# Kernel optimization log

Hardware: AMD Instinct MI355X
Metric: run time of the kernel (lower is better)

## Reference

```python
import jax, jax.numpy as jnp
import numpy as np

LN_EPS = 1e-5

def setup_inputs() -> dict:
    key = jax.random.key(0)
    ks = jax.random.split(key, 8)
    E, N, D, H = 600000, 50000, 128, 512
    edge_attr = jax.random.normal(ks[0], (E, D), dtype=jnp.float32)
    node_feat_src = jax.random.normal(ks[1], (N, D), dtype=jnp.float32)
    node_feat_dst = jax.random.normal(ks[2], (N, D), dtype=jnp.float32)
    edge_index = jax.random.randint(ks[3], (2, E), 0, N, dtype=jnp.int64)
    in_dim = D + 2 * D  # 384
    W1 = jax.random.normal(ks[4], (in_dim, H), dtype=jnp.float32) / np.sqrt(in_dim)
    b1 = jnp.zeros((H,), dtype=jnp.float32)
    g1 = jnp.ones((H,), dtype=jnp.float32)
    be1 = jnp.zeros((H,), dtype=jnp.float32)
    W2 = jax.random.normal(ks[5], (H, D), dtype=jnp.float32) / np.sqrt(H)
    b2 = jnp.zeros((D,), dtype=jnp.float32)
    return dict(edge_attr=edge_attr, node_feat_src=node_feat_src,
                node_feat_dst=node_feat_dst, edge_index=edge_index,
                W1=W1, b1=b1, g1=g1, be1=be1, W2=W2, b2=b2)

def _layer_norm(x, gamma, beta):
    mu = jnp.mean(x, axis=-1, keepdims=True)
    var = jnp.mean(jnp.square(x - mu), axis=-1, keepdims=True)
    return (x - mu) * jax.lax.rsqrt(var + LN_EPS) * gamma + beta

def reference(edge_attr, node_feat_src, node_feat_dst, edge_index,
              W1, b1, g1, be1, W2, b2):
    src_idx, dst_idx = edge_index[0], edge_index[1]
    src_feat = node_feat_src[src_idx]            # [E, node_dim] gather
    dst_feat = node_feat_dst[dst_idx]            # [E, node_dim] gather
    x = jnp.concatenate([edge_attr, src_feat, dst_feat], axis=-1)  # [E, 3D]
    h = x @ W1 + b1                              # [E, H]
    h = jax.nn.silu(_layer_norm(h, g1, be1))
    out = h @ W2 + b2                            # [E, edge_dim]
    return edge_attr + out
```

## Files before the change

### kernel.cpp

```cpp
#include <hip/hip_runtime.h>
#include <hip/hip_bf16.h>


#define E_TOTAL 600000
#define DD      128
#define HH      512
#define IND     384
#define MTILE   64
#define XS      520

typedef __attribute__((ext_vector_type(8))) short bf16x8;
typedef __attribute__((ext_vector_type(4))) float f32x4;

__device__ __forceinline__ ushort f2bf(float f) {
    __hip_bfloat16 b = __float2bfloat16(f);
    return *reinterpret_cast<ushort*>(&b);
}

template <int CTRL>
__device__ __forceinline__ float dpp_add(float x) {
    union { float f; int i; } a, b;
    a.f = x;
    b.i = __builtin_amdgcn_update_dpp(0, a.i, CTRL, 0xf, 0xf, true);
    return x + b.f;
}
__device__ __forceinline__ float row16_sum(float s) {
    s = dpp_add<0xB1>(s);
    s = dpp_add<0x4E>(s);
    s = dpp_add<0x124>(s);
    s = dpp_add<0x128>(s);
    return s;
}

__global__ void prep_weights(const float* __restrict__ W1, const float* __restrict__ W2,
                             ushort* __restrict__ W1t, ushort* __restrict__ W2t) {
    int j = blockIdx.x * 256 + threadIdx.x;
    if (j < IND * HH) {
        int n = j / IND, k = j % IND;
        W1t[j] = f2bf(W1[k * HH + n]);
    }
    int j2 = j - IND * HH;
    if (j2 >= 0 && j2 < HH * DD) {
        int d2 = j2 / HH, k = j2 % HH;
        W2t[j2] = f2bf(W2[k * DD + d2]);
    }
}

__global__ __launch_bounds__(512, 4) void edge_block_kernel(
    const float* __restrict__ edge_attr,
    const float* __restrict__ nsrc,
    const float* __restrict__ ndst,
    const int*   __restrict__ eidx,
    const float* __restrict__ b1,
    const float* __restrict__ g1,
    const float* __restrict__ be1,
    const float* __restrict__ b2,
    const ushort* __restrict__ W1t,
    const ushort* __restrict__ W2t,
    float* __restrict__ out)
{
    __shared__ __align__(16) ushort xbuf[MTILE * XS];
    __shared__ float red_s[MTILE][8];
    __shared__ float red_q[MTILE][8];
    __shared__ __align__(8) float stats[MTILE][2];

    const int tid  = threadIdx.x;
    const int e0   = blockIdx.x * MTILE;
    const int lane = tid & 63;
    const int w    = tid >> 6;
    const int g    = lane >> 4;
    const int li   = lane & 15;

    {
        const int l32 = tid & 31, grp = tid >> 5;
        int si[4], di[4];
        #pragma unroll
        for (int it = 0; it < 4; ++it) {
            const int e = e0 + grp + it * 16;
            si[it] = eidx[e];
            di[it] = eidx[E_TOTAL + e];
        }
        #pragma unroll
        for (int it = 0; it < 4; ++it) {
            const int r = grp + it * 16;
            const int e = e0 + r;
            float4 ea = *(const float4*)&edge_attr[(size_t)e * DD + l32 * 4];
            float4 sf = *(const float4*)&nsrc[(size_t)si[it] * DD + l32 * 4];
            float4 df = *(const float4*)&ndst[(size_t)di[it] * DD + l32 * 4];
            ushort* row = &xbuf[r * XS];
            ushort4 ua = { f2bf(ea.x), f2bf(ea.y), f2bf(ea.z), f2bf(ea.w) };
            ushort4 us = { f2bf(sf.x), f2bf(sf.y), f2bf(sf.z), f2bf(sf.w) };
            ushort4 ud = { f2bf(df.x), f2bf(df.y), f2bf(df.z), f2bf(df.w) };
            *(ushort4*)&row[  0 + l32 * 4] = ua;
            *(ushort4*)&row[128 + l32 * 4] = us;
            *(ushort4*)&row[256 + l32 * 4] = ud;
        }
    }
    __syncthreads();

    const int wn0 = w * 64;
    f32x4 acc[4][4];
    #pragma unroll
    for (int mi = 0; mi < 4; ++mi)
        #pragma unroll
        for (int ni = 0; ni < 4; ++ni)
            acc[mi][ni] = (f32x4){0.f, 0.f, 0.f, 0.f};

    const ushort* w1p = W1t + (size_t)(wn0 + li) * IND + g * 8;

    bf16x8 B1b[2][4];
    #pragma unroll
    for (int ni = 0; ni < 4; ++ni) B1b[0][ni] = *(const bf16x8*)(w1p + ni * 16 * IND);
    #pragma unroll
    for (int ni = 0; ni < 4; ++ni) B1b[1][ni] = *(const bf16x8*)(w1p + ni * 16 * IND + 32);

    #pragma unroll
    for (int kb = 0; kb < 12; ++kb) {
        const int cur = kb & 1;
        const int ko  = kb * 32 + g * 8;
        bf16x8 a[4];
        #pragma unroll
        for (int mi = 0; mi < 4; ++mi)
            a[mi] = *(const bf16x8*)&xbuf[(mi * 16 + li) * XS + ko];
        __builtin_amdgcn_s_setprio(1);
        #pragma unroll
        for (int mi = 0; mi < 4; ++mi)
            #pragma unroll
            for (int ni = 0; ni < 4; ++ni)
                acc[mi][ni] = __builtin_amdgcn_mfma_f32_16x16x32_bf16(
                    a[mi], B1b[cur][ni], acc[mi][ni], 0, 0, 0);
        __builtin_amdgcn_s_setprio(0);
        if (kb < 10) {
            #pragma unroll
            for (int ni = 0; ni < 4; ++ni)
                B1b[cur][ni] = *(const bf16x8*)(w1p + ni * 16 * IND + (kb + 2) * 32);
        }
    }

    float b1v[4], g1v[4], bev[4];
    #pragma unroll
    for (int ni = 0; ni < 4; ++ni) {
        int c = wn0 + ni * 16 + li;
        b1v[ni] = b1[c]; g1v[ni] = g1[c]; bev[ni] = be1[c];
    }

    #pragma unroll
    for (int mi = 0; mi < 4; ++mi) {
        #pragma unroll
        for (int reg = 0; reg < 4; ++reg) {
            float s = 0.f, q = 0.f;
            #pragma unroll
            for (int ni = 0; ni < 4; ++ni) {
                float h = acc[mi][ni][reg] + b1v[ni];
                acc[mi][ni][reg] = h;
                s += h;
                q = fmaf(h, h, q);
            }
            s = row16_sum(s);
            q = row16_sum(q);
            if (li == 0) {
                int row = mi * 16 + g * 4 + reg;
                red_s[row][w] = s;
                red_q[row][w] = q;
            }
        }
    }
    __syncthreads();

    if (tid < MTILE) {
        float s = 0.f, q = 0.f;
        #pragma unroll
        for (int i = 0; i < 8; ++i) { s += red_s[tid][i]; q += red_q[tid][i]; }
        float mu  = s * (1.f / 512.f);
        float var = q * (1.f / 512.f) - mu * mu;
        stats[tid][0] = mu;
        stats[tid][1] = rsqrtf(var + 1e-5f);
    }
    __syncthreads();

    const ushort* w2p = W2t + (size_t)(w * 16 + li) * HH + g * 8;
    bf16x8 B2r[4];
    #pragma unroll
    for (int i = 0; i < 4; ++i) B2r[i] = *(const bf16x8*)(w2p + i * 32);

    #pragma unroll
    for (int mi = 0; mi < 4; ++mi) {
        #pragma unroll
        for (int reg = 0; reg < 4; ++reg) {
            int row = mi * 16 + g * 4 + reg;
            float2 st = *(float2*)&stats[row][0];
            #pragma unroll
            for (int ni = 0; ni < 4; ++ni) {
                float sc = st.y * g1v[ni];
                float tc = fmaf(-st.x, sc, bev[ni]);
                float xn = fmaf(acc[mi][ni][reg], sc, tc);
                float ex = __expf(-xn);
                float a  = xn * __builtin_amdgcn_rcpf(1.f + ex);
                xbuf[row * XS + wn0 + ni * 16 + li] = f2bf(a);
            }
        }
    }
    __syncthreads();

    float ear[8];
    #pragma unroll
    for (int mi = 0; mi < 2; ++mi)
        #pragma unroll
        for (int reg = 0; reg < 4; ++reg) {
            int row = (mi * 2) * 16 + g * 4 + reg;
            ear[mi * 4 + reg] = 0.f;
        }
    float earr[4][4];
    #pragma unroll
    for (int mi = 0; mi < 4; ++mi)
        #pragma unroll
        for (int reg = 0; reg < 4; ++reg) {
            int row = mi * 16 + g * 4 + reg;
            earr[mi][reg] = edge_attr[(size_t)(e0 + row) * DD + w * 16 + li];
        }

    f32x4 acc2[4];
    #pragma unroll
    for (int mi = 0; mi < 4; ++mi) acc2[mi] = (f32x4){0.f, 0.f, 0.f, 0.f};

    #pragma unroll
    for (int kb = 0; kb < 16; ++kb) {
        const int cur = kb & 3;
        bf16x8 bf = B2r[cur];
        if (kb < 12)
            B2r[cur] = *(const bf16x8*)(w2p + (kb + 4) * 32);
        const int ko = kb * 32 + g * 8;
        bf16x8 a2[4];
        #pragma unroll
        for (int mi = 0; mi < 4; ++mi)
            a2[mi] = *(const bf16x8*)&xbuf[(mi * 16 + li) * XS + ko];
        __builtin_amdgcn_s_setprio(1);
        #pragma unroll
        for (int mi = 0; mi < 4; ++mi)
            acc2[mi] = __builtin_amdgcn_mfma_f32_16x16x32_bf16(a2[mi], bf, acc2[mi], 0, 0, 0);
        __builtin_amdgcn_s_setprio(0);
    }

    const float b2v = b2[w * 16 + li];
    #pragma unroll
    for (int mi = 0; mi < 4; ++mi) {
        #pragma unroll
        for (int reg = 0; reg < 4; ++reg) {
            int row = mi * 16 + g * 4 + reg;
            size_t o = (size_t)(e0 + row) * DD + w * 16 + li;
            out[o] = acc2[mi][reg] + b2v + earr[mi][reg];
        }
    }
    (void)ear;
}

extern "C" void kernel_launch(void* const* d_in, const int* in_sizes, int n_in,
                              void* d_out, int out_size, void* d_ws, size_t ws_size,
                              hipStream_t stream) {
    const float* edge_attr = (const float*)d_in[0];
    const float* nsrc      = (const float*)d_in[1];
    const float* ndst      = (const float*)d_in[2];
    const int*   eidx      = (const int*)d_in[3];
    const float* W1        = (const float*)d_in[4];
    const float* b1        = (const float*)d_in[5];
    const float* g1        = (const float*)d_in[6];
    const float* be1       = (const float*)d_in[7];
    const float* W2        = (const float*)d_in[8];
    const float* b2        = (const float*)d_in[9];
    float* out = (float*)d_out;

    ushort* W1t = (ushort*)d_ws;
    ushort* W2t = W1t + IND * HH;

    hipLaunchKernelGGL(prep_weights,
                       dim3((IND * HH + HH * DD + 255) / 256), dim3(256), 0, stream,
                       W1, W2, W1t, W2t);

    hipLaunchKernelGGL(edge_block_kernel,
                       dim3(E_TOTAL / MTILE), dim3(512), 0, stream,
                       edge_attr, nsrc, ndst, eidx, b1, g1, be1, b2, W1t, W2t, out);
}
```

Measured before the change: 665.4 us.

## Switch both GEMMs to 32x32x16 MFMA with a 2x4 warp tiling

Replaces the 16x16x32 bf16 MFMA tiles with 32x32x16 tiles and reorganises the 8 waves into a 2x4 (M x N) grid. Each wave now computes 32 rows by 128 columns in GEMM1 and 32 rows by 32 columns in GEMM2, with A fragments double-buffered from LDS. The intent is fewer LDS reads per FLOP and higher MFMA efficiency. The LayerNorm reduction indexing and the output mapping are rewritten to match the new accumulator layout, which carries a risk of indexing errors. Lowering the per-wave tile to 32 rows also changes how much the W2 fragment loads are reused.

```diff
diff --git a/kernel.cpp b/kernel.cpp
--- a/kernel.cpp
+++ b/kernel.cpp
@@ -9,8 +9,8 @@
 #define MTILE   64
 #define XS      520
 
-typedef __attribute__((ext_vector_type(8))) short bf16x8;
-typedef __attribute__((ext_vector_type(4))) float f32x4;
+typedef __attribute__((ext_vector_type(8)))  short bf16x8;
+typedef __attribute__((ext_vector_type(16))) float f32x16;
 
 __device__ __forceinline__ ushort f2bf(float f) {
     __hip_bfloat16 b = __float2bfloat16(f);
@@ -68,8 +68,11 @@
     const int e0   = blockIdx.x * MTILE;
     const int lane = tid & 63;
     const int w    = tid >> 6;
-    const int g    = lane >> 4;
-    const int li   = lane & 15;
+    const int l31  = lane & 31;
+    const int hi   = lane >> 5;
+    const int hi2  = (lane >> 4) & 1;
+    const int wm   = w >> 2;
+    const int wn   = w & 3;
 
     {
         const int l32 = tid & 31, grp = tid >> 5;
@@ -98,71 +101,65 @@
     }
     __syncthreads();
 
-    const int wn0 = w * 64;
-    f32x4 acc[4][4];
-    #pragma unroll
-    for (int mi = 0; mi < 4; ++mi)
-        #pragma unroll
-        for (int ni = 0; ni < 4; ++ni)
-            acc[mi][ni] = (f32x4){0.f, 0.f, 0.f, 0.f};
-
-    const ushort* w1p = W1t + (size_t)(wn0 + li) * IND + g * 8;
-
-    bf16x8 B1b[2][4];
-    #pragma unroll
-    for (int ni = 0; ni < 4; ++ni) B1b[0][ni] = *(const bf16x8*)(w1p + ni * 16 * IND);
-    #pragma unroll
-    for (int ni = 0; ni < 4; ++ni) B1b[1][ni] = *(const bf16x8*)(w1p + ni * 16 * IND + 32);
-
-    #pragma unroll
-    for (int kb = 0; kb < 12; ++kb) {
-        const int cur = kb & 1;
-        const int ko  = kb * 32 + g * 8;
-        bf16x8 a[4];
-        #pragma unroll
-        for (int mi = 0; mi < 4; ++mi)
-            a[mi] = *(const bf16x8*)&xbuf[(mi * 16 + li) * XS + ko];
+    f32x16 acc[4];
+    #pragma unroll
+    for (int nf = 0; nf < 4; ++nf)
+        #pragma unroll
+        for (int r = 0; r < 16; ++r) acc[nf][r] = 0.f;
+
+    const ushort* w1p = W1t + (size_t)(wn * 128 + l31) * IND + hi * 8;
+    const ushort* xrow = &xbuf[(wm * 32 + l31) * XS + hi * 8];
+
+    bf16x8 B1r[2][4];
+    #pragma unroll
+    for (int nf = 0; nf < 4; ++nf) B1r[0][nf] = *(const bf16x8*)(w1p + nf * 32 * IND);
+    #pragma unroll
+    for (int nf = 0; nf < 4; ++nf) B1r[1][nf] = *(const bf16x8*)(w1p + nf * 32 * IND + 16);
+
+    bf16x8 a_[2];
+    a_[0] = *(const bf16x8*)(xrow);
+
+    #pragma unroll
+    for (int ks = 0; ks < 24; ++ks) {
+        const int cur = ks & 1;
+        if (ks < 23)
+            a_[cur ^ 1] = *(const bf16x8*)(xrow + (ks + 1) * 16);
         __builtin_amdgcn_s_setprio(1);
         #pragma unroll
-        for (int mi = 0; mi < 4; ++mi)
+        for (int nf = 0; nf < 4; ++nf)
+            acc[nf] = __builtin_amdgcn_mfma_f32_32x32x16_bf16(
+                a_[cur], B1r[cur][nf], acc[nf], 0, 0, 0);
+        __builtin_amdgcn_s_setprio(0);
+        if (ks < 22) {
             #pragma unroll
-            for (int ni = 0; ni < 4; ++ni)
-                acc[mi][ni] = __builtin_amdgcn_mfma_f32_16x16x32_bf16(
-                    a[mi], B1b[cur][ni], acc[mi][ni], 0, 0, 0);
-        __builtin_amdgcn_s_setprio(0);
-        if (kb < 10) {
-            #pragma unroll
-            for (int ni = 0; ni < 4; ++ni)
-                B1b[cur][ni] = *(const bf16x8*)(w1p + ni * 16 * IND + (kb + 2) * 32);
+            for (int nf = 0; nf < 4; ++nf)
+                B1r[cur][nf] = *(const bf16x8*)(w1p + nf * 32 * IND + (ks + 2) * 16);
         }
     }
 
     float b1v[4], g1v[4], bev[4];
     #pragma unroll
-    for (int ni = 0; ni < 4; ++ni) {
-        int c = wn0 + ni * 16 + li;
-        b1v[ni] = b1[c]; g1v[ni] = g1[c]; bev[ni] = be1[c];
-    }
-
-    #pragma unroll
-    for (int mi = 0; mi < 4; ++mi) {
-        #pragma unroll
-        for (int reg = 0; reg < 4; ++reg) {
-            float s = 0.f, q = 0.f;
-            #pragma unroll
-            for (int ni = 0; ni < 4; ++ni) {
-                float h = acc[mi][ni][reg] + b1v[ni];
-                acc[mi][ni][reg] = h;
-                s += h;
-                q = fmaf(h, h, q);
-            }
-            s = row16_sum(s);
-            q = row16_sum(q);
-            if (li == 0) {
-                int row = mi * 16 + g * 4 + reg;
-                red_s[row][w] = s;
-                red_q[row][w] = q;
-            }
+    for (int nf = 0; nf < 4; ++nf) {
+        int c = wn * 128 + nf * 32 + l31;
+        b1v[nf] = b1[c]; g1v[nf] = g1[c]; bev[nf] = be1[c];
+    }
+
+    #pragma unroll
+    for (int reg = 0; reg < 16; ++reg) {
+        float s = 0.f, q = 0.f;
+        #pragma unroll
+        for (int nf = 0; nf < 4; ++nf) {
+            float h = acc[nf][reg] + b1v[nf];
+            acc[nf][reg] = h;
+            s += h;
+            q = fmaf(h, h, q);
+        }
+        s = row16_sum(s);
+        q = row16_sum(q);
+        if ((lane & 15) == 0) {
+            int row = wm * 32 + (reg & 3) + 8 * (reg >> 2) + 4 * hi;
+            red_s[row][wn * 2 + hi2] = s;
+            red_q[row][wn * 2 + hi2] = q;
         }
     }
     __syncthreads();
@@ -178,80 +175,59 @@
     }
     __syncthreads();
 
-    const ushort* w2p = W2t + (size_t)(w * 16 + li) * HH + g * 8;
+    #pragma unroll
+    for (int reg = 0; reg < 16; ++reg) {
+        int row = wm * 32 + (reg & 3) + 8 * (reg >> 2) + 4 * hi;
+        float2 st = *(float2*)&stats[row][0];
+        #pragma unroll
+        for (int nf = 0; nf < 4; ++nf) {
+            float sc = st.y * g1v[nf];
+            float tc = fmaf(-st.x, sc, bev[nf]);
+            float xn = fmaf(acc[nf][reg], sc, tc);
+            float av = xn * __builtin_amdgcn_rcpf(1.f + __expf(-xn));
+            xbuf[row * XS + wn * 128 + nf * 32 + l31] = f2bf(av);
+        }
+    }
+
+    float earr[16];
+    #pragma unroll
+    for (int reg = 0; reg < 16; ++reg) {
+        int row = wm * 32 + (reg & 3) + 8 * (reg >> 2) + 4 * hi;
+        earr[reg] = edge_attr[(size_t)(e0 + row) * DD + wn * 32 + l31];
+    }
+    __syncthreads();
+
+    const ushort* w2p = W2t + (size_t)(wn * 32 + l31) * HH + hi * 8;
+    const ushort* arow2 = &xbuf[(wm * 32 + l31) * XS + hi * 8];
+
     bf16x8 B2r[4];
     #pragma unroll
-    for (int i = 0; i < 4; ++i) B2r[i] = *(const bf16x8*)(w2p + i * 32);
-
-    #pragma unroll
-    for (int mi = 0; mi < 4; ++mi) {
-        #pragma unroll
-        for (int reg = 0; reg < 4; ++reg) {
-            int row = mi * 16 + g * 4 + reg;
-            float2 st = *(float2*)&stats[row][0];
-            #pragma unroll
-            for (int ni = 0; ni < 4; ++ni) {
-                float sc = st.y * g1v[ni];
-                float tc = fmaf(-st.x, sc, bev[ni]);
-                float xn = fmaf(acc[mi][ni][reg], sc, tc);
-                float ex = __expf(-xn);
-                float a  = xn * __builtin_amdgcn_rcpf(1.f + ex);
-                xbuf[row * XS + wn0 + ni * 16 + li] = f2bf(a);
-            }
-        }
-    }
-    __syncthreads();
-
-    float ear[8];
-    #pragma unroll
-    for (int mi = 0; mi < 2; ++mi)
-        #pragma unroll
-        for (int reg = 0; reg < 4; ++reg) {
-            int row = (mi * 2) * 16 + g * 4 + reg;
-            ear[mi * 4 + reg] = 0.f;
-        }
-    float earr[4][4];
-    #pragma unroll
-    for (int mi = 0; mi < 4; ++mi)
-        #pragma unroll
-        for (int reg = 0; reg < 4; ++reg) {
-            int row = mi * 16 + g * 4 + reg;
-            earr[mi][reg] = edge_attr[(size_t)(e0 + row) * DD + w * 16 + li];
-        }
-
-    f32x4 acc2[4];
-    #pragma unroll
-    for (int mi = 0; mi < 4; ++mi) acc2[mi] = (f32x4){0.f, 0.f, 0.f, 0.f};
-
-    #pragma unroll
-    for (int kb = 0; kb < 16; ++kb) {
-        const int cur = kb & 3;
-        bf16x8 bf = B2r[cur];
-        if (kb < 12)
-            B2r[cur] = *(const bf16x8*)(w2p + (kb + 4) * 32);
-        const int ko = kb * 32 + g * 8;
-        bf16x8 a2[4];
-        #pragma unroll
-        for (int mi = 0; mi < 4; ++mi)
-            a2[mi] = *(const bf16x8*)&xbuf[(mi * 16 + li) * XS + ko];
-        __builtin_amdgcn_s_setprio(1);
-        #pragma unroll
-        for (int mi = 0; mi < 4; ++mi)
-            acc2[mi] = __builtin_amdgcn_mfma_f32_16x16x32_bf16(a2[mi], bf, acc2[mi], 0, 0, 0);
-        __builtin_amdgcn_s_setprio(0);
-    }
-
-    const float b2v = b2[w * 16 + li];
-    #pragma unroll
-    for (int mi = 0; mi < 4; ++mi) {
-        #pragma unroll
-        for (int reg = 0; reg < 4; ++reg) {
-            int row = mi * 16 + g * 4 + reg;
-            size_t o = (size_t)(e0 + row) * DD + w * 16 + li;
-            out[o] = acc2[mi][reg] + b2v + earr[mi][reg];
-        }
-    }
-    (void)ear;
+    for (int i = 0; i < 4; ++i) B2r[i] = *(const bf16x8*)(w2p + i * 16);
+
+    f32x16 acc2;
+    #pragma unroll
+    for (int r = 0; r < 16; ++r) acc2[r] = 0.f;
+
+    bf16x8 a2_[2];
+    a2_[0] = *(const bf16x8*)(arow2);
+
+    #pragma unroll
+    for (int ks = 0; ks < 32; ++ks) {
+        const int cur = ks & 1;
+        if (ks < 31)
+            a2_[cur ^ 1] = *(const bf16x8*)(arow2 + (ks + 1) * 16);
+        acc2 = __builtin_amdgcn_mfma_f32_32x32x16_bf16(a2_[cur], B2r[ks & 3], acc2, 0, 0, 0);
+        if (ks < 28)
+            B2r[ks & 3] = *(const bf16x8*)(w2p + (ks + 4) * 16);
+    }
+
+    const float b2v = b2[wn * 32 + l31];
+    #pragma unroll
+    for (int reg = 0; reg < 16; ++reg) {
+        int row = wm * 32 + (reg & 3) + 8 * (reg >> 2) + 4 * hi;
+        size_t o = (size_t)(e0 + row) * DD + wn * 32 + l31;
+        out[o] = acc2[reg] + b2v + earr[reg];
+    }
 }
 
 extern "C" void kernel_launch(void* const* d_in, const int* in_sizes, int n_in,
```

Result: slower. 1.214 ms (+82.5%).

## Replace padded LDS rows with XOR-swizzled layout and hoist epilogue loads

Applied to the files above, without the earlier changes.

The padded shared-memory row stride (520) is replaced by unpadded rows of 384 (first GEMM) and 512 (second GEMM), using an XOR swizzle of 8-element chunks keyed on the row to avoid bank conflicts. This cuts LDS footprint from 66.5KB to 64KB per block, which may ease occupancy. The edge_attr residual loads and W2 fragment prefetch are moved earlier, before the LayerNorm reduction barrier, so their latency overlaps the stats computation. Swizzle indexing adds some integer ALU work and must stay consistent between writers and readers.

```diff
diff --git a/kernel.cpp b/kernel.cpp
--- a/kernel.cpp
+++ b/kernel.cpp
@@ -7,7 +7,6 @@
 #define HH      512
 #define IND     384
 #define MTILE   64
-#define XS      520
 
 typedef __attribute__((ext_vector_type(8))) short bf16x8;
 typedef __attribute__((ext_vector_type(4))) float f32x4;
@@ -59,7 +58,7 @@
     const ushort* __restrict__ W2t,
     float* __restrict__ out)
 {
-    __shared__ __align__(16) ushort xbuf[MTILE * XS];
+    __shared__ __align__(16) ushort xbuf[MTILE * 512];
     __shared__ float red_s[MTILE][8];
     __shared__ float red_q[MTILE][8];
     __shared__ __align__(8) float stats[MTILE][2];
@@ -70,6 +69,7 @@
     const int w    = tid >> 6;
     const int g    = lane >> 4;
     const int li   = lane & 15;
+    const int sx   = li & 7;
 
     {
         const int l32 = tid & 31, grp = tid >> 5;
@@ -80,20 +80,23 @@
             si[it] = eidx[e];
             di[it] = eidx[E_TOTAL + e];
         }
+        const int ch = l32 >> 1;
+        const int off8 = (l32 & 1) * 4;
         #pragma unroll
         for (int it = 0; it < 4; ++it) {
             const int r = grp + it * 16;
             const int e = e0 + r;
+            const int rs = r & 7;
             float4 ea = *(const float4*)&edge_attr[(size_t)e * DD + l32 * 4];
             float4 sf = *(const float4*)&nsrc[(size_t)si[it] * DD + l32 * 4];
             float4 df = *(const float4*)&ndst[(size_t)di[it] * DD + l32 * 4];
-            ushort* row = &xbuf[r * XS];
+            ushort* row = &xbuf[r * IND];
             ushort4 ua = { f2bf(ea.x), f2bf(ea.y), f2bf(ea.z), f2bf(ea.w) };
             ushort4 us = { f2bf(sf.x), f2bf(sf.y), f2bf(sf.z), f2bf(sf.w) };
             ushort4 ud = { f2bf(df.x), f2bf(df.y), f2bf(df.z), f2bf(df.w) };
-            *(ushort4*)&row[  0 + l32 * 4] = ua;
-            *(ushort4*)&row[128 + l32 * 4] = us;
-            *(ushort4*)&row[256 + l32 * 4] = ud;
+            *(ushort4*)&row[(((ch     ) ^ rs) << 3) + off8] = ua;
+            *(ushort4*)&row[(((ch + 16) ^ rs) << 3) + off8] = us;
+            *(ushort4*)&row[(((ch + 32) ^ rs) << 3) + off8] = ud;
         }
     }
     __syncthreads();
@@ -117,11 +120,11 @@
     #pragma unroll
     for (int kb = 0; kb < 12; ++kb) {
         const int cur = kb & 1;
-        const int ko  = kb * 32 + g * 8;
+        const int swc = ((kb * 4 + g) ^ sx) << 3;
         bf16x8 a[4];
         #pragma unroll
         for (int mi = 0; mi < 4; ++mi)
-            a[mi] = *(const bf16x8*)&xbuf[(mi * 16 + li) * XS + ko];
+            a[mi] = *(const bf16x8*)&xbuf[(mi * 16 + li) * IND + swc];
         __builtin_amdgcn_s_setprio(1);
         #pragma unroll
         for (int mi = 0; mi < 4; ++mi)
@@ -165,7 +168,21 @@
             }
         }
     }
-    __syncthreads();
+
+    float earr[4][4];
+    #pragma unroll
+    for (int mi = 0; mi < 4; ++mi)
+        #pragma unroll
+        for (int reg = 0; reg < 4; ++reg) {
+            int row = mi * 16 + g * 4 + reg;
+            earr[mi][reg] = edge_attr[(size_t)(e0 + row) * DD + w * 16 + li];
+        }
+    __syncthreads();
+
+    const ushort* w2p = W2t + (size_t)(w * 16 + li) * HH + g * 8;
+    bf16x8 B2r[4];
+    #pragma unroll
+    for (int i = 0; i < 4; ++i) B2r[i] = *(const bf16x8*)(w2p + i * 32);
 
     if (tid < MTILE) {
         float s = 0.f, q = 0.f;
@@ -178,46 +195,27 @@
     }
     __syncthreads();
 
-    const ushort* w2p = W2t + (size_t)(w * 16 + li) * HH + g * 8;
-    bf16x8 B2r[4];
-    #pragma unroll
-    for (int i = 0; i < 4; ++i) B2r[i] = *(const bf16x8*)(w2p + i * 32);
-
     #pragma unroll
     for (int mi = 0; mi < 4; ++mi) {
         #pragma unroll
         for (int reg = 0; reg < 4; ++reg) {
             int row = mi * 16 + g * 4 + reg;
+            int rs  = row & 7;
             float2 st = *(float2*)&stats[row][0];
+            ushort* arow = &xbuf[row * HH];
             #pragma unroll
             for (int ni = 0; ni < 4; ++ni) {
                 float sc = st.y * g1v[ni];
                 float tc = fmaf(-st.x, sc, bev[ni]);
                 float xn = fmaf(acc[mi][ni][reg], sc, tc);
                 float ex = __expf(-xn);
-                float a  = xn * __builtin_amdgcn_rcpf(1.f + ex);
-                xbuf[row * XS + wn0 + ni * 16 + li] = f2bf(a);
+                float av = xn * __builtin_amdgcn_rcpf(1.f + ex);
+                int col = wn0 + ni * 16 + li;
+                arow[(((col >> 3) ^ rs) << 3) + (col & 7)] = f2bf(av);
             }
         }
     }
     __syncthreads();
-
-    float ear[8];
-    #pragma unroll
-    for (int mi = 0; mi < 2; ++mi)
-        #pragma unroll
-        for (int reg = 0; reg < 4; ++reg) {
-            int row = (mi * 2) * 16 + g * 4 + reg;
-            ear[mi * 4 + reg] = 0.f;
-        }
-    float earr[4][4];
-    #pragma unroll
-    for (int mi = 0; mi < 4; ++mi)
-        #pragma unroll
-        for (int reg = 0; reg < 4; ++reg) {
-            int row = mi * 16 + g * 4 + reg;
-            earr[mi][reg] = edge_attr[(size_t)(e0 + row) * DD + w * 16 + li];
-        }
 
     f32x4 acc2[4];
     #pragma unroll
@@ -229,11 +227,11 @@
         bf16x8 bf = B2r[cur];
         if (kb < 12)
             B2r[cur] = *(const bf16x8*)(w2p + (kb + 4) * 32);
-        const int ko = kb * 32 + g * 8;
+        const int swc = ((kb * 4 + g) ^ sx) << 3;
         bf16x8 a2[4];
         #pragma unroll
         for (int mi = 0; mi < 4; ++mi)
-            a2[mi] = *(const bf16x8*)&xbuf[(mi * 16 + li) * XS + ko];
+            a2[mi] = *(const bf16x8*)&xbuf[(mi * 16 + li) * HH + swc];
         __builtin_amdgcn_s_setprio(1);
         #pragma unroll
         for (int mi = 0; mi < 4; ++mi)
@@ -251,7 +249,6 @@
             out[o] = acc2[mi][reg] + b2v + earr[mi][reg];
         }
     }
-    (void)ear;
 }
 
 extern "C" void kernel_launch(void* const* d_in, const int* in_sizes, int n_in,
```

Result: slower. 937.8 us (+40.9%).
